# Kernel optimization log

Measured on AMD Instinct MI355X. Metric: run time of the kernel, lower is better.

Reference implementation:

```python
import jax, jax.numpy as jnp
import numpy as np

DIM, HEADS, DIM_HEAD, DY_DIM = 256, 8, 64, 16
INNER = HEADS * DIM_HEAD
B, N = 4, 1024
EPS = 1e-5


def _leaky(x):
    return jnp.where(x >= 0, x, 0.01 * x)


def _gelu(x):
    return jax.nn.gelu(x, approximate=False)  # torch nn.GELU default (erf)


def setup_inputs() -> dict:
    key = jax.random.key(0)
    ks = jax.random.split(key, 14)

    def lin(k, fan_in, fan_out):
        bound = 1.0 / np.sqrt(fan_in)
        return jax.random.uniform(k, (fan_in, fan_out), jnp.float32, -bound, bound)

    return {
        "xyzs": jax.random.normal(ks[0], (B, N, 3), jnp.float32),
        "features": jax.random.normal(ks[1], (B, N, DIM), jnp.float32),
        "gamma": jnp.ones((DIM,), jnp.float32),
        "beta": jnp.zeros((DIM,), jnp.float32),
        "W_qkv": lin(ks[2], DIM, 3 * INNER),
        "W_pos1": lin(ks[3], 3, DY_DIM),
        "W_pos2": lin(ks[4], DY_DIM, 3),
        "W_neg1": lin(ks[5], 3, DY_DIM),
        "W_neg2": lin(ks[6], DY_DIM, 3),
        "W_cross": lin(ks[7], 3, 3),
        "b_cross": jax.random.uniform(ks[8], (3,), jnp.float32, -0.5, 0.5),
        "W_spatial": lin(ks[9], 3, DIM_HEAD),
        "W_out": lin(ks[10], INNER, DIM),
        "b_out": jax.random.uniform(ks[11], (DIM,), jnp.float32, -1.0 / np.sqrt(INNER), 1.0 / np.sqrt(INNER)),
    }


def reference(xyzs, features, gamma, beta, W_qkv, W_pos1, W_pos2, W_neg1, W_neg2,
              W_cross, b_cross, W_spatial, W_out, b_out):
    b, n, dim = features.shape
    d = W_spatial.shape[1]                       # dim_head
    h = W_qkv.shape[1] // (3 * d)                # heads
    scale = d ** -0.5

    # LayerNorm
    mu = jnp.mean(features, axis=-1, keepdims=True)
    var = jnp.var(features, axis=-1, keepdims=True)
    x = (features - mu) * jax.lax.rsqrt(var + EPS) * gamma + beta

    # qkv projection -> (b, h, n, d)
    qkv = x @ W_qkv                              # (b, n, 3*h*d)
    q, k, v = jnp.split(qkv, 3, axis=-1)
    to_bhnd = lambda t: t.reshape(b, n, h, d).transpose(0, 2, 1, 3)
    q, k, v = to_bhnd(q), to_bhnd(k), to_bhnd(v)

    # pairwise deltas: delta[b, i, j] = xyzs[b, j] - xyzs[b, i]  (b, n, n, 3)
    delta = xyzs[:, None, :, :] - xyzs[:, :, None, :]

    pos = _leaky(_gelu(jax.nn.relu(delta) @ W_pos1) @ W_pos2)
    neg = _leaky(_gelu(jax.nn.relu(-delta) @ W_neg1) @ W_neg2)
    cross = _leaky((pos * neg) @ W_cross + b_cross)
    delta = cross * delta                        # (b, n, n, 3)

    # full softmax attention
    dots = jnp.einsum('bhid,bhjd->bhij', q, k) * scale
    attn = jax.nn.softmax(dots, axis=-1)         # (b, h, n, n)

    v_out = jnp.einsum('bhij,bhjd->bhid', attn, v)
    # attention-weighted reduction of pairwise deltas (no (b,h,n,n,3) materialization)
    wdelta = jnp.einsum('bhij,bijc->bhic', attn, delta)   # (b, h, n, 3)
    disp = wdelta @ W_spatial                    # (b, h, n, d)

    out = (v_out + disp).transpose(0, 2, 1, 3).reshape(b, n, h * d)
    out = _gelu(out @ W_out + b_out)             # to_out: Linear + GELU (dropout=0)
    return out + features
```

## Files before the change

kernel.cpp:

```cpp
#include <hip/hip_runtime.h>
#include <hip/hip_bf16.h>
#include <math.h>

#define BB 4
#define NN 1024
#define DIMM 256
#define HEADS 8
#define DH 64
#define INNERD 512
#define NT 16
#define MDPLANE 4194304

typedef __bf16 bf16x8 __attribute__((ext_vector_type(8)));
typedef float f32x4 __attribute__((ext_vector_type(4)));

__device__ __forceinline__ float gelu_poly(float x) {
    float xc = fminf(fmaxf(x, -3.0f), 3.0f);
    float u = xc * xc;
    float f = fmaf(u, fmaf(u, fmaf(u, fmaf(u, 4.4413e-5f, -1.33195e-3f),
                                   1.70980e-2f), -1.299964e-1f), 7.9734583e-1f);
    float E = xc * f;
    float hx = 0.5f * xc;
    float g = fmaf(hx, E, hx);
    return g + fmaxf(x - 3.0f, 0.0f);
}
__device__ __forceinline__ float leaky_f(float x) {
    return fmaxf(x, 0.01f * x);
}

__global__ __launch_bounds__(256) void ln_kernel(const float* __restrict__ feat,
                                                 const float* __restrict__ gamma,
                                                 const float* __restrict__ beta,
                                                 __hip_bfloat16* __restrict__ xb) {
    int row = blockIdx.x;
    int t = threadIdx.x;
    float v = feat[row * DIMM + t];
    float s = v, ss = v * v;
    #pragma unroll
    for (int off = 1; off < 64; off <<= 1) {
        s += __shfl_xor(s, off);
        ss += __shfl_xor(ss, off);
    }
    __shared__ float red[2][4];
    int w = t >> 6, lane = t & 63;
    if (lane == 0) { red[0][w] = s; red[1][w] = ss; }
    __syncthreads();
    s = red[0][0] + red[0][1] + red[0][2] + red[0][3];
    ss = red[1][0] + red[1][1] + red[1][2] + red[1][3];
    float mu = s * (1.0f / DIMM);
    float var = ss * (1.0f / DIMM) - mu * mu;
    float rs = rsqrtf(var + 1e-5f);
    xb[row * DIMM + t] = __float2bfloat16((v - mu) * rs * gamma[t] + beta[t]);
}

__global__ __launch_bounds__(256) void wtg_kernel(const float* __restrict__ W,
                                                  __hip_bfloat16* __restrict__ Wt,
                                                  int C, int R) {
    __shared__ float tile[64][65];
    int n0 = blockIdx.x * 64, k0 = blockIdx.y * 64;
    int tid = threadIdx.x;
    int cc = tid & 63, rr = tid >> 6;
    #pragma unroll
    for (int p = 0; p < 16; ++p) {
        int k = rr + p * 4;
        tile[k][cc] = W[(k0 + k) * C + n0 + cc];
    }
    __syncthreads();
    #pragma unroll
    for (int p = 0; p < 16; ++p) {
        int n = rr + p * 4;
        Wt[(n0 + n) * R + k0 + cc] = __float2bfloat16(tile[cc][n]);
    }
}

__device__ __forceinline__ void qkv_body(int bx,
                                         const __hip_bfloat16* __restrict__ xb,
                                         const __hip_bfloat16* __restrict__ Wt,
                                         __hip_bfloat16* __restrict__ qb,
                                         __hip_bfloat16* __restrict__ kb,
                                         __hip_bfloat16* __restrict__ vtb) {
    int mt = bx & 63, nt = bx >> 6;
    int tid = threadIdx.x, w = tid >> 6, lane = tid & 63;
    int g = lane >> 4, c = lane & 15;

    const __hip_bfloat16* ap = xb + (mt * 64 + w * 16 + c) * 256 + g * 8;
    bf16x8 a[8];
    #pragma unroll
    for (int ks = 0; ks < 8; ++ks) a[ks] = *reinterpret_cast<const bf16x8*>(ap + ks * 32);

    f32x4 acc[4];
    #pragma unroll
    for (int jf = 0; jf < 4; ++jf) { acc[jf][0] = 0.f; acc[jf][1] = 0.f; acc[jf][2] = 0.f; acc[jf][3] = 0.f; }

    const __hip_bfloat16* bp = Wt + (nt * 64 + c) * 256 + g * 8;
    #pragma unroll
    for (int jf = 0; jf < 4; ++jf) {
        const __hip_bfloat16* bpj = bp + jf * 16 * 256;
        #pragma unroll
        for (int ks = 0; ks < 8; ++ks) {
            bf16x8 bfrag = *reinterpret_cast<const bf16x8*>(bpj + ks * 32);
            acc[jf] = __builtin_amdgcn_mfma_f32_16x16x32_bf16(a[ks], bfrag, acc[jf], 0, 0, 0);
        }
    }

    int col0 = nt * 64;
    int part = col0 >> 9;
    int h = (col0 >> 6) & 7;
    #pragma unroll
    for (int jf = 0; jf < 4; ++jf) {
        int d = jf * 16 + c;
        #pragma unroll
        for (int r = 0; r < 4; ++r) {
            int m = mt * 64 + w * 16 + g * 4 + r;
            int b = m >> 10, nn = m & 1023;
            if (part == 0)
                qb[(((b * HEADS + h) * NN) + nn) * DH + d] = __float2bfloat16(acc[jf][r] * 0.125f);
            else if (part == 1)
                kb[(((b * HEADS + h) * NN) + nn) * DH + d] = __float2bfloat16(acc[jf][r]);
            else
                vtb[((long)(b * HEADS + h) * DH + d) * NN + nn] = __float2bfloat16(acc[jf][r]);
        }
    }
}

__device__ __forceinline__ void dmlp_body(int bi,
                                          const float* __restrict__ xyz,
                                          const float* __restrict__ Wp1,
                                          const float* __restrict__ Wp2,
                                          const float* __restrict__ Wn1,
                                          const float* __restrict__ Wn2,
                                          const float* __restrict__ Wc,
                                          const float* __restrict__ bc,
                                          __hip_bfloat16* __restrict__ md) {
    int tid = threadIdx.x;
    int b = bi >> 10;
    const float* xj = xyz + (long)b * NN * 3;
    float xi0 = xyz[bi * 3 + 0], xi1 = xyz[bi * 3 + 1], xi2 = xyz[bi * 3 + 2];

    float d0[4], d1[4], d2[4];
    #pragma unroll
    for (int p = 0; p < 4; ++p) {
        int j = tid + p * 256;
        d0[p] = xj[j * 3 + 0] - xi0;
        d1[p] = xj[j * 3 + 1] - xi1;
        d2[p] = xj[j * 3 + 2] - xi2;
    }

    float pp0[4], pp1[4], pp2[4], nv0[4], nv1[4], nv2[4];
    {
        float r0[4], r1[4], r2[4];
        float a0[4] = {}, a1[4] = {}, a2[4] = {};
        #pragma unroll
        for (int p = 0; p < 4; ++p) {
            r0[p] = fmaxf(d0[p], 0.f); r1[p] = fmaxf(d1[p], 0.f); r2[p] = fmaxf(d2[p], 0.f);
        }
        #pragma unroll
        for (int m = 0; m < 16; ++m) {
            float w0 = Wp1[m], w1 = Wp1[16 + m], w2 = Wp1[32 + m];
            float u0 = Wp2[3 * m], u1 = Wp2[3 * m + 1], u2 = Wp2[3 * m + 2];
            #pragma unroll
            for (int p = 0; p < 4; ++p) {
                float t = fmaf(r0[p], w0, fmaf(r1[p], w1, r2[p] * w2));
                t = gelu_poly(t);
                a0[p] = fmaf(t, u0, a0[p]);
                a1[p] = fmaf(t, u1, a1[p]);
                a2[p] = fmaf(t, u2, a2[p]);
            }
        }
        #pragma unroll
        for (int p = 0; p < 4; ++p) {
            pp0[p] = leaky_f(a0[p]); pp1[p] = leaky_f(a1[p]); pp2[p] = leaky_f(a2[p]);
        }
    }
    {
        float r0[4], r1[4], r2[4];
        float a0[4] = {}, a1[4] = {}, a2[4] = {};
        #pragma unroll
        for (int p = 0; p < 4; ++p) {
            r0[p] = fmaxf(-d0[p], 0.f); r1[p] = fmaxf(-d1[p], 0.f); r2[p] = fmaxf(-d2[p], 0.f);
        }
        #pragma unroll
        for (int m = 0; m < 16; ++m) {
            float w0 = Wn1[m], w1 = Wn1[16 + m], w2 = Wn1[32 + m];
            float u0 = Wn2[3 * m], u1 = Wn2[3 * m + 1], u2 = Wn2[3 * m + 2];
            #pragma unroll
            for (int p = 0; p < 4; ++p) {
                float t = fmaf(r0[p], w0, fmaf(r1[p], w1, r2[p] * w2));
                t = gelu_poly(t);
                a0[p] = fmaf(t, u0, a0[p]);
                a1[p] = fmaf(t, u1, a1[p]);
                a2[p] = fmaf(t, u2, a2[p]);
            }
        }
        #pragma unroll
        for (int p = 0; p < 4; ++p) {
            nv0[p] = leaky_f(a0[p]); nv1[p] = leaky_f(a1[p]); nv2[p] = leaky_f(a2[p]);
        }
    }
    float c00 = Wc[0], c01 = Wc[1], c02 = Wc[2];
    float c10 = Wc[3], c11 = Wc[4], c12 = Wc[5];
    float c20 = Wc[6], c21 = Wc[7], c22 = Wc[8];
    float b0 = bc[0], b1 = bc[1], b2 = bc[2];

    long base = (long)bi * NN;
    #pragma unroll
    for (int p = 0; p < 4; ++p) {
        int j = tid + p * 256;
        float q0 = pp0[p] * nv0[p], q1 = pp1[p] * nv1[p], q2 = pp2[p] * nv2[p];
        float c0 = leaky_f(fmaf(q0, c00, fmaf(q1, c10, fmaf(q2, c20, b0))));
        float c1 = leaky_f(fmaf(q0, c01, fmaf(q1, c11, fmaf(q2, c21, b1))));
        float c2 = leaky_f(fmaf(q0, c02, fmaf(q1, c12, fmaf(q2, c22, b2))));
        md[base + j]               = __float2bfloat16(c0 * d0[p]);
        md[MDPLANE + base + j]     = __float2bfloat16(c1 * d1[p]);
        md[2 * MDPLANE + base + j] = __float2bfloat16(c2 * d2[p]);
    }
}

__global__ __launch_bounds__(256) void fused_mid(const float* __restrict__ xyz,
                                                 const float* __restrict__ Wp1,
                                                 const float* __restrict__ Wp2,
                                                 const float* __restrict__ Wn1,
                                                 const float* __restrict__ Wn2,
                                                 const float* __restrict__ Wc,
                                                 const float* __restrict__ bc,
                                                 __hip_bfloat16* __restrict__ md,
                                                 const __hip_bfloat16* __restrict__ xb,
                                                 const __hip_bfloat16* __restrict__ Wt,
                                                 __hip_bfloat16* __restrict__ qb,
                                                 __hip_bfloat16* __restrict__ kb,
                                                 __hip_bfloat16* __restrict__ vtb) {
    int bx = blockIdx.x;
    if (bx < 4096)
        dmlp_body(bx, xyz, Wp1, Wp2, Wn1, Wn2, Wc, bc, md);
    else
        qkv_body(bx - 4096, xb, Wt, qb, kb, vtb);
}

__global__ __launch_bounds__(256) void attn_kernel(
    const __hip_bfloat16* __restrict__ q,
    const __hip_bfloat16* __restrict__ kk,
    const __hip_bfloat16* __restrict__ vt,
    const __hip_bfloat16* __restrict__ md,
    const float* __restrict__ Wsp,
    __hip_bfloat16* __restrict__ yb)
{
    int it = blockIdx.x, h = blockIdx.y, b = blockIdx.z;
    int tid = threadIdx.x;
    int w = tid >> 6, lane = tid & 63;
    int g = lane >> 4, c = lane & 15;

    __shared__ __align__(16) __hip_bfloat16 k_lds[2][64][64];
    __shared__ __align__(16) __hip_bfloat16 v_lds[2][64][64];
    __shared__ __align__(16) __hip_bfloat16 p_lds[4][16][64];

    const __hip_bfloat16* qp = q + ((long)(b * HEADS + h) * NN + it * 64) * DH;
    const __hip_bfloat16* kp = kk + (long)(b * HEADS + h) * NN * DH;
    const __hip_bfloat16* vp = vt + (long)(b * HEADS + h) * DH * NN;

    bf16x8 qa[2];
    #pragma unroll
    for (int t2 = 0; t2 < 2; ++t2)
        qa[t2] = *reinterpret_cast<const bf16x8*>(qp + (w * 16 + c) * DH + t2 * 32 + g * 8);

    int r0 = tid >> 3;
    int d00 = (tid & 7) * 8;
    int4 kreg[2], vreg[2];

    f32x4 o[4];
    #pragma unroll
    for (int df = 0; df < 4; ++df) { o[df][0] = 0.f; o[df][1] = 0.f; o[df][2] = 0.f; o[df][3] = 0.f; }
    float m_[4] = {-1e30f, -1e30f, -1e30f, -1e30f};
    float l_[4] = {0.f, 0.f, 0.f, 0.f};
    float wdx[4] = {0.f, 0.f, 0.f, 0.f}, wdy[4] = {0.f, 0.f, 0.f, 0.f}, wdz[4] = {0.f, 0.f, 0.f, 0.f};

    #pragma unroll
    for (int c2 = 0; c2 < 2; ++c2) {
        int r = r0 + c2 * 32;
        kreg[c2] = *reinterpret_cast<const int4*>(kp + (0 * 64 + r) * DH + d00);
        vreg[c2] = *reinterpret_cast<const int4*>(vp + (long)r * NN + 0 * 64 + d00);
    }
    #pragma unroll
    for (int c2 = 0; c2 < 2; ++c2) {
        int r = r0 + c2 * 32;
        int sd = d00 ^ ((r & 7) << 3);
        *reinterpret_cast<int4*>(&k_lds[0][r][sd]) = kreg[c2];
        *reinterpret_cast<int4*>(&v_lds[0][r][sd]) = vreg[c2];
    }
    __syncthreads();

    const __hip_bfloat16* md0 = md;
    const __hip_bfloat16* md1 = md + MDPLANE;
    const __hip_bfloat16* md2 = md + 2 * MDPLANE;
    long mdrow = (long)(b * NN + it * 64 + w * 16 + g * 4) * NN + c;

    for (int t = 0; t < NT; ++t) {
        int buf = t & 1;
        if (t + 1 < NT) {
            #pragma unroll
            for (int c2 = 0; c2 < 2; ++c2) {
                int r = r0 + c2 * 32;
                kreg[c2] = *reinterpret_cast<const int4*>(kp + ((t + 1) * 64 + r) * DH + d00);
                vreg[c2] = *reinterpret_cast<const int4*>(vp + (long)r * NN + (t + 1) * 64 + d00);
            }
        }

        float mdc[4][4][3];
        #pragma unroll
        for (int r = 0; r < 4; ++r) {
            long off = mdrow + (long)r * NN + t * 64;
            #pragma unroll
            for (int jf = 0; jf < 4; ++jf) {
                mdc[r][jf][0] = __bfloat162float(md0[off + jf * 16]);
                mdc[r][jf][1] = __bfloat162float(md1[off + jf * 16]);
                mdc[r][jf][2] = __bfloat162float(md2[off + jf * 16]);
            }
        }

        f32x4 s[4];
        #pragma unroll
        for (int jf = 0; jf < 4; ++jf) {
            f32x4 acc = {0.f, 0.f, 0.f, 0.f};
            int jl = jf * 16 + c;
            int sw = (jl & 7) << 3;
            #pragma unroll
            for (int t2 = 0; t2 < 2; ++t2) {
                bf16x8 bk = *reinterpret_cast<const bf16x8*>(&k_lds[buf][jl][(t2 * 32 + g * 8) ^ sw]);
                acc = __builtin_amdgcn_mfma_f32_16x16x32_bf16(qa[t2], bk, acc, 0, 0, 0);
            }
            s[jf] = acc;
        }

        float pe[4][4];
        #pragma unroll
        for (int r = 0; r < 4; ++r) {
            float tm = fmaxf(fmaxf(s[0][r], s[1][r]), fmaxf(s[2][r], s[3][r]));
            tm = fmaxf(tm, __shfl_xor(tm, 1));
            tm = fmaxf(tm, __shfl_xor(tm, 2));
            tm = fmaxf(tm, __shfl_xor(tm, 4));
            tm = fmaxf(tm, __shfl_xor(tm, 8));
            float nm = fmaxf(m_[r], tm);
            float corr = __expf(m_[r] - nm);
            m_[r] = nm;
            l_[r] *= corr;
            wdx[r] *= corr; wdy[r] *= corr; wdz[r] *= corr;
            o[0][r] *= corr; o[1][r] *= corr; o[2][r] *= corr; o[3][r] *= corr;
            float ps = 0.f;
            #pragma unroll
            for (int jf = 0; jf < 4; ++jf) {
                float p = __expf(s[jf][r] - nm);
                pe[r][jf] = p;
                ps += p;
            }
            l_[r] += ps;
        }

        #pragma unroll
        for (int r = 0; r < 4; ++r) {
            int row = g * 4 + r;
            int sw = (row & 7) << 3;
            #pragma unroll
            for (int jf = 0; jf < 4; ++jf)
                p_lds[w][row][(jf * 16 + c) ^ sw] = __float2bfloat16(pe[r][jf]);
        }
        asm volatile("s_waitcnt lgkmcnt(0)" ::: "memory");

        #pragma unroll
        for (int r = 0; r < 4; ++r) {
            #pragma unroll
            for (int jf = 0; jf < 4; ++jf) {
                wdx[r] = fmaf(pe[r][jf], mdc[r][jf][0], wdx[r]);
                wdy[r] = fmaf(pe[r][jf], mdc[r][jf][1], wdy[r]);
                wdz[r] = fmaf(pe[r][jf], mdc[r][jf][2], wdz[r]);
            }
        }

        #pragma unroll
        for (int t2 = 0; t2 < 2; ++t2) {
            int swp = (c & 7) << 3;
            bf16x8 pa = *reinterpret_cast<const bf16x8*>(&p_lds[w][c][(t2 * 32 + g * 8) ^ swp]);
            #pragma unroll
            for (int df = 0; df < 4; ++df) {
                int dl = df * 16 + c;
                int swv = (dl & 7) << 3;
                bf16x8 bv = *reinterpret_cast<const bf16x8*>(&v_lds[buf][dl][(t2 * 32 + g * 8) ^ swv]);
                o[df] = __builtin_amdgcn_mfma_f32_16x16x32_bf16(pa, bv, o[df], 0, 0, 0);
            }
        }

        if (t + 1 < NT) {
            #pragma unroll
            for (int c2 = 0; c2 < 2; ++c2) {
                int r = r0 + c2 * 32;
                int sd = d00 ^ ((r & 7) << 3);
                *reinterpret_cast<int4*>(&k_lds[buf ^ 1][r][sd]) = kreg[c2];
                *reinterpret_cast<int4*>(&v_lds[buf ^ 1][r][sd]) = vreg[c2];
            }
        }
        __syncthreads();
    }

    #pragma unroll
    for (int r = 0; r < 4; ++r) {
        float lv = l_[r];
        lv += __shfl_xor(lv, 1); lv += __shfl_xor(lv, 2);
        lv += __shfl_xor(lv, 4); lv += __shfl_xor(lv, 8);
        float w0 = wdx[r], w1 = wdy[r], w2 = wdz[r];
        w0 += __shfl_xor(w0, 1); w0 += __shfl_xor(w0, 2); w0 += __shfl_xor(w0, 4); w0 += __shfl_xor(w0, 8);
        w1 += __shfl_xor(w1, 1); w1 += __shfl_xor(w1, 2); w1 += __shfl_xor(w1, 4); w1 += __shfl_xor(w1, 8);
        w2 += __shfl_xor(w2, 1); w2 += __shfl_xor(w2, 2); w2 += __shfl_xor(w2, 4); w2 += __shfl_xor(w2, 8);
        float inv = 1.0f / lv;
        w0 *= inv; w1 *= inv; w2 *= inv;
        int row = g * 4 + r;
        long ig = (long)b * NN + it * 64 + w * 16 + row;
        __hip_bfloat16* yp = yb + ig * INNERD + h * DH;
        #pragma unroll
        for (int df = 0; df < 4; ++df) {
            int d = df * 16 + c;
            float disp = w0 * Wsp[d] + w1 * Wsp[64 + d] + w2 * Wsp[128 + d];
            yp[d] = __float2bfloat16(o[df][r] * inv + disp);
        }
    }
}

__global__ __launch_bounds__(256) void out_gemm(const __hip_bfloat16* __restrict__ yb,
                                                const __hip_bfloat16* __restrict__ Wot,
                                                const float* __restrict__ bout,
                                                const float* __restrict__ feat,
                                                float* __restrict__ out) {
    int mt = blockIdx.x, nt = blockIdx.y;
    int tid = threadIdx.x, w = tid >> 6, lane = tid & 63;
    int g = lane >> 4, c = lane & 15;

    const __hip_bfloat16* ap = yb + ((long)mt * 64 + w * 16 + c) * INNERD + g * 8;
    bf16x8 a[16];
    #pragma unroll
    for (int ks = 0; ks < 16; ++ks) a[ks] = *reinterpret_cast<const bf16x8*>(ap + ks * 32);

    f32x4 acc[4];
    #pragma unroll
    for (int jf = 0; jf < 4; ++jf) { acc[jf][0] = 0.f; acc[jf][1] = 0.f; acc[jf][2] = 0.f; acc[jf][3] = 0.f; }

    const __hip_bfloat16* bp = Wot + (nt * 64 + c) * INNERD + g * 8;
    #pragma unroll
    for (int jf = 0; jf < 4; ++jf) {
        const __hip_bfloat16* bpj = bp + jf * 16 * INNERD;
        #pragma unroll
        for (int ks = 0; ks < 16; ++ks) {
            bf16x8 bfrag = *reinterpret_cast<const bf16x8*>(bpj + ks * 32);
            acc[jf] = __builtin_amdgcn_mfma_f32_16x16x32_bf16(a[ks], bfrag, acc[jf], 0, 0, 0);
        }
    }

    #pragma unroll
    for (int jf = 0; jf < 4; ++jf) {
        int d = nt * 64 + jf * 16 + c;
        float bo = bout[d];
        #pragma unroll
        for (int r = 0; r < 4; ++r) {
            long m = (long)mt * 64 + w * 16 + g * 4 + r;
            float val = gelu_poly(acc[jf][r] + bo);
            out[m * DIMM + d] = val + feat[m * DIMM + d];
        }
    }
}

extern "C" void kernel_launch(void* const* d_in, const int* in_sizes, int n_in,
                              void* d_out, int out_size, void* d_ws, size_t ws_size,
                              hipStream_t stream) {
    const float* xyzs  = (const float*)d_in[0];
    const float* feat  = (const float*)d_in[1];
    const float* gamma = (const float*)d_in[2];
    const float* beta  = (const float*)d_in[3];
    const float* Wqkv  = (const float*)d_in[4];
    const float* Wp1   = (const float*)d_in[5];
    const float* Wp2   = (const float*)d_in[6];
    const float* Wn1   = (const float*)d_in[7];
    const float* Wn2   = (const float*)d_in[8];
    const float* Wc    = (const float*)d_in[9];
    const float* bc    = (const float*)d_in[10];
    const float* Wsp   = (const float*)d_in[11];
    const float* Wout  = (const float*)d_in[12];
    const float* bout  = (const float*)d_in[13];
    float* out = (float*)d_out;

    __hip_bfloat16* xb  = (__hip_bfloat16*)d_ws;
    __hip_bfloat16* Wt  = xb + 1048576;
    __hip_bfloat16* Wot = Wt + 393216;
    __hip_bfloat16* qb  = Wot + 131072;
    __hip_bfloat16* kb  = qb + 2097152;
    __hip_bfloat16* vtb = kb + 2097152;
    __hip_bfloat16* yb  = vtb + 2097152;
    __hip_bfloat16* md  = yb + 2097152;

    ln_kernel<<<4096, 256, 0, stream>>>(feat, gamma, beta, xb);
    wtg_kernel<<<dim3(24, 4), 256, 0, stream>>>(Wqkv, Wt, 1536, 256);
    wtg_kernel<<<dim3(4, 8), 256, 0, stream>>>(Wout, Wot, 256, 512);
    fused_mid<<<5632, 256, 0, stream>>>(xyzs, Wp1, Wp2, Wn1, Wn2, Wc, bc, md,
                                        xb, Wt, qb, kb, vtb);
    attn_kernel<<<dim3(16, HEADS, BB), 256, 0, stream>>>(qb, kb, vtb, md, Wsp, yb);
    out_gemm<<<dim3(64, 4), 256, 0, stream>>>(yb, Wot, bout, feat, out);
}
```

Baseline: 134.3 us.

## Merge prep kernels, stage delta-MLP weights in LDS, use fast GELU and fp16 deltas

Folds the LayerNorm kernel and both weight-transpose launches into a single prep kernel to cut launch overhead. In the delta-MLP blocks, the small MLP weights are copied into shared memory once per block, and the clamped polynomial GELU is replaced with a tanh-style approximation built on __expf and a fast divide. The weighted delta buffer is now stored as fp16 instead of bf16, which costs the same bandwidth but keeps more mantissa bits. The tanh-form GELU departs slightly from the exact erf GELU the reference uses.

```diff
diff --git a/kernel.cpp b/kernel.cpp
--- a/kernel.cpp
+++ b/kernel.cpp
@@ -24,52 +24,73 @@
     float g = fmaf(hx, E, hx);
     return g + fmaxf(x - 3.0f, 0.0f);
 }
+
+__device__ __forceinline__ float gelu_fast(float x) {
+    float x2 = x * x;
+    float z = x * fmaf(x2, 0.0356774081f, 0.7978845608f);
+    float e = __expf(-2.0f * z);
+    return __fdividef(x, 1.0f + e);
+}
 __device__ __forceinline__ float leaky_f(float x) {
     return fmaxf(x, 0.01f * x);
 }
 
-__global__ __launch_bounds__(256) void ln_kernel(const float* __restrict__ feat,
-                                                 const float* __restrict__ gamma,
-                                                 const float* __restrict__ beta,
-                                                 __hip_bfloat16* __restrict__ xb) {
-    int row = blockIdx.x;
-    int t = threadIdx.x;
-    float v = feat[row * DIMM + t];
-    float s = v, ss = v * v;
-    #pragma unroll
-    for (int off = 1; off < 64; off <<= 1) {
-        s += __shfl_xor(s, off);
-        ss += __shfl_xor(ss, off);
-    }
-    __shared__ float red[2][4];
-    int w = t >> 6, lane = t & 63;
-    if (lane == 0) { red[0][w] = s; red[1][w] = ss; }
-    __syncthreads();
-    s = red[0][0] + red[0][1] + red[0][2] + red[0][3];
-    ss = red[1][0] + red[1][1] + red[1][2] + red[1][3];
-    float mu = s * (1.0f / DIMM);
-    float var = ss * (1.0f / DIMM) - mu * mu;
-    float rs = rsqrtf(var + 1e-5f);
-    xb[row * DIMM + t] = __float2bfloat16((v - mu) * rs * gamma[t] + beta[t]);
-}
-
-__global__ __launch_bounds__(256) void wtg_kernel(const float* __restrict__ W,
-                                                  __hip_bfloat16* __restrict__ Wt,
-                                                  int C, int R) {
-    __shared__ float tile[64][65];
-    int n0 = blockIdx.x * 64, k0 = blockIdx.y * 64;
+__global__ __launch_bounds__(256) void prep_kernel(const float* __restrict__ feat,
+                                                   const float* __restrict__ gamma,
+                                                   const float* __restrict__ beta,
+                                                   __hip_bfloat16* __restrict__ xb,
+                                                   const float* __restrict__ Wqkv,
+                                                   __hip_bfloat16* __restrict__ Wt,
+                                                   const float* __restrict__ Wout,
+                                                   __hip_bfloat16* __restrict__ Wot) {
+    __shared__ float smem[64 * 65];
+    int bx = blockIdx.x;
     int tid = threadIdx.x;
-    int cc = tid & 63, rr = tid >> 6;
-    #pragma unroll
-    for (int p = 0; p < 16; ++p) {
-        int k = rr + p * 4;
-        tile[k][cc] = W[(k0 + k) * C + n0 + cc];
-    }
-    __syncthreads();
-    #pragma unroll
-    for (int p = 0; p < 16; ++p) {
-        int n = rr + p * 4;
-        Wt[(n0 + n) * R + k0 + cc] = __float2bfloat16(tile[cc][n]);
+    if (bx < 4096) {
+        int row = bx;
+        float v = feat[row * DIMM + tid];
+        float s = v, ss = v * v;
+        #pragma unroll
+        for (int off = 1; off < 64; off <<= 1) {
+            s += __shfl_xor(s, off);
+            ss += __shfl_xor(ss, off);
+        }
+        float* red = smem;
+        int w = tid >> 6, lane = tid & 63;
+        if (lane == 0) { red[w] = s; red[4 + w] = ss; }
+        __syncthreads();
+        s = red[0] + red[1] + red[2] + red[3];
+        ss = red[4] + red[5] + red[6] + red[7];
+        float mu = s * (1.0f / DIMM);
+        float var = ss * (1.0f / DIMM) - mu * mu;
+        float rs = rsqrtf(var + 1e-5f);
+        xb[row * DIMM + tid] = __float2bfloat16((v - mu) * rs * gamma[tid] + beta[tid]);
+    } else {
+        const float* W;
+        __hip_bfloat16* Wd;
+        int C, R, nx, ky;
+        if (bx < 4192) {
+            int t = bx - 4096;
+            W = Wqkv; Wd = Wt; C = 1536; R = 256;
+            nx = t % 24; ky = t / 24;
+        } else {
+            int t = bx - 4192;
+            W = Wout; Wd = Wot; C = 256; R = 512;
+            nx = t % 4; ky = t / 4;
+        }
+        int n0 = nx * 64, k0 = ky * 64;
+        int cc = tid & 63, rr = tid >> 6;
+        #pragma unroll
+        for (int p = 0; p < 16; ++p) {
+            int k = rr + p * 4;
+            smem[k * 65 + cc] = W[(k0 + k) * C + n0 + cc];
+        }
+        __syncthreads();
+        #pragma unroll
+        for (int p = 0; p < 16; ++p) {
+            int n = rr + p * 4;
+            Wd[(n0 + n) * R + k0 + cc] = __float2bfloat16(smem[cc * 65 + n]);
+        }
     }
 }
 
@@ -125,13 +146,8 @@
 
 __device__ __forceinline__ void dmlp_body(int bi,
                                           const float* __restrict__ xyz,
-                                          const float* __restrict__ Wp1,
-                                          const float* __restrict__ Wp2,
-                                          const float* __restrict__ Wn1,
-                                          const float* __restrict__ Wn2,
-                                          const float* __restrict__ Wc,
-                                          const float* __restrict__ bc,
-                                          __hip_bfloat16* __restrict__ md) {
+                                          const float* __restrict__ w,
+                                          _Float16* __restrict__ md) {
     int tid = threadIdx.x;
     int b = bi >> 10;
     const float* xj = xyz + (long)b * NN * 3;
@@ -156,12 +172,12 @@
         }
         #pragma unroll
         for (int m = 0; m < 16; ++m) {
-            float w0 = Wp1[m], w1 = Wp1[16 + m], w2 = Wp1[32 + m];
-            float u0 = Wp2[3 * m], u1 = Wp2[3 * m + 1], u2 = Wp2[3 * m + 2];
+            float w0 = w[m], w1 = w[16 + m], w2 = w[32 + m];
+            float u0 = w[48 + 3 * m], u1 = w[48 + 3 * m + 1], u2 = w[48 + 3 * m + 2];
             #pragma unroll
             for (int p = 0; p < 4; ++p) {
                 float t = fmaf(r0[p], w0, fmaf(r1[p], w1, r2[p] * w2));
-                t = gelu_poly(t);
+                t = gelu_fast(t);
                 a0[p] = fmaf(t, u0, a0[p]);
                 a1[p] = fmaf(t, u1, a1[p]);
                 a2[p] = fmaf(t, u2, a2[p]);
@@ -181,12 +197,12 @@
         }
         #pragma unroll
         for (int m = 0; m < 16; ++m) {
-            float w0 = Wn1[m], w1 = Wn1[16 + m], w2 = Wn1[32 + m];
-            float u0 = Wn2[3 * m], u1 = Wn2[3 * m + 1], u2 = Wn2[3 * m + 2];
+            float w0 = w[96 + m], w1 = w[96 + 16 + m], w2 = w[96 + 32 + m];
+            float u0 = w[144 + 3 * m], u1 = w[144 + 3 * m + 1], u2 = w[144 + 3 * m + 2];
             #pragma unroll
             for (int p = 0; p < 4; ++p) {
                 float t = fmaf(r0[p], w0, fmaf(r1[p], w1, r2[p] * w2));
-                t = gelu_poly(t);
+                t = gelu_fast(t);
                 a0[p] = fmaf(t, u0, a0[p]);
                 a1[p] = fmaf(t, u1, a1[p]);
                 a2[p] = fmaf(t, u2, a2[p]);
@@ -197,11 +213,14 @@
             nv0[p] = leaky_f(a0[p]); nv1[p] = leaky_f(a1[p]); nv2[p] = leaky_f(a2[p]);
         }
     }
-    float c00 = Wc[0], c01 = Wc[1], c02 = Wc[2];
-    float c10 = Wc[3], c11 = Wc[4], c12 = Wc[5];
-    float c20 = Wc[6], c21 = Wc[7], c22 = Wc[8];
-    float b0 = bc[0], b1 = bc[1], b2 = bc[2];
-
+    float c00 = w[192], c01 = w[193], c02 = w[194];
+    float c10 = w[195], c11 = w[196], c12 = w[197];
+    float c20 = w[198], c21 = w[199], c22 = w[200];
+    float b0 = w[201], b1 = w[202], b2 = w[203];
+
+    _Float16* st0 = md;
+    _Float16* st1 = md + MDPLANE;
+    _Float16* st2 = md + 2 * MDPLANE;
     long base = (long)bi * NN;
     #pragma unroll
     for (int p = 0; p < 4; ++p) {
@@ -210,9 +229,9 @@
         float c0 = leaky_f(fmaf(q0, c00, fmaf(q1, c10, fmaf(q2, c20, b0))));
         float c1 = leaky_f(fmaf(q0, c01, fmaf(q1, c11, fmaf(q2, c21, b1))));
         float c2 = leaky_f(fmaf(q0, c02, fmaf(q1, c12, fmaf(q2, c22, b2))));
-        md[base + j]               = __float2bfloat16(c0 * d0[p]);
-        md[MDPLANE + base + j]     = __float2bfloat16(c1 * d1[p]);
-        md[2 * MDPLANE + base + j] = __float2bfloat16(c2 * d2[p]);
+        st0[base + j] = (_Float16)(c0 * d0[p]);
+        st1[base + j] = (_Float16)(c1 * d1[p]);
+        st2[base + j] = (_Float16)(c2 * d2[p]);
     }
 }
 
@@ -223,24 +242,38 @@
                                                  const float* __restrict__ Wn2,
                                                  const float* __restrict__ Wc,
                                                  const float* __restrict__ bc,
-                                                 __hip_bfloat16* __restrict__ md,
+                                                 _Float16* __restrict__ md,
                                                  const __hip_bfloat16* __restrict__ xb,
                                                  const __hip_bfloat16* __restrict__ Wt,
                                                  __hip_bfloat16* __restrict__ qb,
                                                  __hip_bfloat16* __restrict__ kb,
                                                  __hip_bfloat16* __restrict__ vtb) {
+    __shared__ float wlds[204];
     int bx = blockIdx.x;
-    if (bx < 4096)
-        dmlp_body(bx, xyz, Wp1, Wp2, Wn1, Wn2, Wc, bc, md);
-    else
+    if (bx < 4096) {
+        int t = threadIdx.x;
+        if (t < 204) {
+            float v;
+            if (t < 48) v = Wp1[t];
+            else if (t < 96) v = Wp2[t - 48];
+            else if (t < 144) v = Wn1[t - 96];
+            else if (t < 192) v = Wn2[t - 144];
+            else if (t < 201) v = Wc[t - 192];
+            else v = bc[t - 201];
+            wlds[t] = v;
+        }
+        __syncthreads();
+        dmlp_body(bx, xyz, wlds, md);
+    } else {
         qkv_body(bx - 4096, xb, Wt, qb, kb, vtb);
+    }
 }
 
 __global__ __launch_bounds__(256) void attn_kernel(
     const __hip_bfloat16* __restrict__ q,
     const __hip_bfloat16* __restrict__ kk,
     const __hip_bfloat16* __restrict__ vt,
-    const __hip_bfloat16* __restrict__ md,
+    const _Float16* __restrict__ md,
     const float* __restrict__ Wsp,
     __hip_bfloat16* __restrict__ yb)
 {
@@ -288,9 +321,9 @@
     }
     __syncthreads();
 
-    const __hip_bfloat16* md0 = md;
-    const __hip_bfloat16* md1 = md + MDPLANE;
-    const __hip_bfloat16* md2 = md + 2 * MDPLANE;
+    const _Float16* md0 = md;
+    const _Float16* md1 = md + MDPLANE;
+    const _Float16* md2 = md + 2 * MDPLANE;
     long mdrow = (long)(b * NN + it * 64 + w * 16 + g * 4) * NN + c;
 
     for (int t = 0; t < NT; ++t) {
@@ -310,9 +343,9 @@
             long off = mdrow + (long)r * NN + t * 64;
             #pragma unroll
             for (int jf = 0; jf < 4; ++jf) {
-                mdc[r][jf][0] = __bfloat162float(md0[off + jf * 16]);
-                mdc[r][jf][1] = __bfloat162float(md1[off + jf * 16]);
-                mdc[r][jf][2] = __bfloat162float(md2[off + jf * 16]);
+                mdc[r][jf][0] = (float)md0[off + jf * 16];
+                mdc[r][jf][1] = (float)md1[off + jf * 16];
+                mdc[r][jf][2] = (float)md2[off + jf * 16];
             }
         }
 
@@ -490,11 +523,9 @@
     __hip_bfloat16* kb  = qb + 2097152;
     __hip_bfloat16* vtb = kb + 2097152;
     __hip_bfloat16* yb  = vtb + 2097152;
-    __hip_bfloat16* md  = yb + 2097152;
-
-    ln_kernel<<<4096, 256, 0, stream>>>(feat, gamma, beta, xb);
-    wtg_kernel<<<dim3(24, 4), 256, 0, stream>>>(Wqkv, Wt, 1536, 256);
-    wtg_kernel<<<dim3(4, 8), 256, 0, stream>>>(Wout, Wot, 256, 512);
+    _Float16* md = (_Float16*)(yb + 2097152);
+
+    prep_kernel<<<4224, 256, 0, stream>>>(feat, gamma, beta, xb, Wqkv, Wt, Wout, Wot);
     fused_mid<<<5632, 256, 0, stream>>>(xyzs, Wp1, Wp2, Wn1, Wn2, Wc, bc, md,
                                         xb, Wt, qb, kb, vtb);
     attn_kernel<<<dim3(16, HEADS, BB), 256, 0, stream>>>(qb, kb, vtb, md, Wsp, yb);
```

New measurement: 172.4 us. 1.28x slower.
